# Performance work log

Measured on AMD Instinct MI355X. Metric: run time of the kernel, lower is better.

Reference implementation:

```python
import jax, jax.numpy as jnp
import numpy as np
import math

L = 16
LOGT = 19
T = 2 ** LOGT
F = 2
NMIN = 16
NMAX = 2048
X_MIN = 0.0
X_MAX = 1.0
N_POINTS = 524288
P1 = np.uint32(2654435761)  # spatial hash prime for y
P2 = np.uint32(805459861)   # spatial hash prime for z


def setup_inputs() -> dict:
    key = jax.random.key(0)
    k1, k2 = jax.random.split(key)
    x = jax.random.uniform(k1, (N_POINTS, 3), dtype=jnp.float32)
    hashmap = jax.random.normal(k2, (L, T, F), dtype=jnp.float32) * 1e-2
    b = math.exp((math.log(NMAX) - math.log(NMIN)) / (L - 1))
    resolution = jnp.asarray(np.floor(NMIN * b ** np.arange(L)), dtype=jnp.float32)
    return {"x": x, "hashmap": hashmap, "resolution": resolution}


def reference(x, hashmap, resolution):
    # normalize coords to [0,1] (x_min=0, x_max=1 here)
    xn = (x - X_MIN) / (X_MAX - X_MIN)
    # per-level scaled coords: [L, n, 3]
    xs = xn[None, :, :] * resolution[:, None, None]
    x0f = jnp.floor(xs)
    w = xs - x0f                                 # trilinear weights [L, n, 3]
    c0 = x0f.astype(jnp.uint32)
    c1 = c0 + jnp.uint32(1)
    hx0, hy0, hz0 = c0[..., 0], c0[..., 1] * P1, c0[..., 2] * P2
    hx1, hy1, hz1 = c1[..., 0], c1[..., 1] * P1, c1[..., 2] * P2
    Tm = jnp.uint32(T - 1)
    # 8 corner hash indices, order 000,001,010,011,100,101,110,111: [L, n, 8]
    idx = jnp.stack([
        (hx0 ^ hy0 ^ hz0) & Tm, (hx0 ^ hy0 ^ hz1) & Tm,
        (hx0 ^ hy1 ^ hz0) & Tm, (hx0 ^ hy1 ^ hz1) & Tm,
        (hx1 ^ hy0 ^ hz0) & Tm, (hx1 ^ hy0 ^ hz1) & Tm,
        (hx1 ^ hy1 ^ hz0) & Tm, (hx1 ^ hy1 ^ hz1) & Tm,
    ], axis=-1).astype(jnp.int32)
    wx, wy, wz = w[..., 0], w[..., 1], w[..., 2]
    wxn, wyn, wzn = 1.0 - wx, 1.0 - wy, 1.0 - wz
    # corner weights matching idx order: [L, n, 8]
    cw = jnp.stack([
        wxn * wyn * wzn, wxn * wyn * wz, wxn * wy * wzn, wxn * wy * wz,
        wx * wyn * wzn, wx * wyn * wz, wx * wy * wzn, wx * wy * wz,
    ], axis=-1)
    # gather per-level corner features: [L, n, 8, F]
    feats = jax.vmap(lambda h, i: h[i])(hashmap, idx)
    # interpolate and lay out as [n, L*F] (level-major, matching kernel store)
    out = jnp.einsum('lnc,lncf->nlf', cw, feats)
    return out.reshape(x.shape[0], L * F)
```

## Files before the change

kernel.cpp:

```cpp
#include <hip/hip_runtime.h>

namespace {
constexpr unsigned kT  = 1u << 19;
constexpr unsigned kTm = kT - 1u;
constexpr unsigned kP1 = 2654435761u;
constexpr unsigned kP2 = 805459861u;
constexpr int      kNPTS = 524288;

constexpr int      kD[3]    = {17, 23, 31};
constexpr unsigned kC[3]    = {17u*17u*17u, 23u*23u*23u, 31u*31u*31u};
constexpr unsigned kBase[3] = {0u, kC[0]*8u, (kC[0]+kC[1])*8u};
constexpr unsigned kTotElems = (kC[0]+kC[1]+kC[2])*8u;
constexpr size_t   kStageOff   = (size_t)4u << 20;
constexpr size_t   kStageBytes = (size_t)kNPTS * 16u * 8u;
constexpr size_t   kWsNeed     = kStageOff + kStageBytes;

constexpr int kNSeg[8]      = {5,2,3,3,2,3,3,2};
constexpr int kSegLvl[8][5] = {
  {0,1,2,3,4}, {4,5,0,0,0}, {5,6,7,0,0}, {7,8,9,0,0},
  {9,10,0,0,0}, {10,11,12,0,0}, {12,13,14,0,0}, {14,15,0,0,0}};
constexpr int kSegBeg[8][5] = {
  {0,0,0,0,0}, {26,0,0,0,0}, {1485,0,0,0,0}, {896,0,0,0,0},
  {307,0,0,0,0}, {1766,0,0,0,0}, {1177,0,0,0,0}, {589,0,0,0,0}};
constexpr int kSegEnd[8][5] = {
  {2048,2048,2048,2048,26}, {2048,1485,0,0,0}, {2048,2048,896,0,0},
  {2048,2048,307,0,0}, {2048,1766,0,0,0}, {2048,2048,1177,0,0},
  {2048,2048,589,0,0}, {2048,2048,0,0,0}};
constexpr unsigned kMaxBlk = 8218;
}

typedef float f32x2 __attribute__((ext_vector_type(2)));
typedef float f32x4 __attribute__((ext_vector_type(4)));

__global__ __launch_bounds__(256) void build_dense(
    const float* __restrict__ hashmap, f32x2* __restrict__ dense)
{
    unsigned t = blockIdx.x * 256 + threadIdx.x;
    if (t >= kTotElems) return;
    int l; unsigned rem;
    if (t < kC[0]*8u)              { l = 0; rem = t; }
    else if (t < (kC[0]+kC[1])*8u) { l = 1; rem = t - kC[0]*8u; }
    else                           { l = 2; rem = t - (kC[0]+kC[1])*8u; }
    unsigned cell = rem >> 3, corner = rem & 7u;
    unsigned D = (unsigned)kD[l];
    unsigned ck = cell % D, tmp = cell / D;
    unsigned cj = tmp % D,  ci = tmp / D;
    unsigned ii = ci + ((corner >> 2) & 1u);
    unsigned jj = cj + ((corner >> 1) & 1u);
    unsigned kk = ck + (corner & 1u);
    unsigned h = (ii ^ (jj * kP1) ^ (kk * kP2)) & kTm;
    dense[t] = reinterpret_cast<const f32x2*>(hashmap)[(size_t)l * kT + h];
}

__global__ __launch_bounds__(256) void hashgrid_gather(
    const float* __restrict__ x,
    const float* __restrict__ hashmap,
    const float* __restrict__ resolution,
    const f32x2* __restrict__ dense,
    f32x2* __restrict__ stage)
{
    unsigned i = blockIdx.x;
    unsigned g = i & 7u;
    unsigned j = i >> 3;

    int lvl = -1; unsigned chunk = 0, acc = 0;
    #pragma unroll
    for (int s = 0; s < 5; ++s) {
        if (s >= kNSeg[g]) break;
        unsigned len = (unsigned)(kSegEnd[g][s] - kSegBeg[g][s]);
        if (j < acc + len) { lvl = kSegLvl[g][s]; chunk = kSegBeg[g][s] + (j - acc); break; }
        acc += len;
    }
    if (lvl < 0) return;

    int n = (int)(chunk * 256u + threadIdx.x);

    float px = __builtin_nontemporal_load(&x[3*n+0]);
    float py = __builtin_nontemporal_load(&x[3*n+1]);
    float pz = __builtin_nontemporal_load(&x[3*n+2]);
    float res = resolution[lvl];

    float xs = px*res, ys = py*res, zs = pz*res;
    float fx = floorf(xs), fy = floorf(ys), fz = floorf(zs);
    float wx = xs-fx, wy = ys-fy, wz = zs-fz;

    unsigned cx0 = (unsigned)fx;
    unsigned cy0 = (unsigned)fy;
    unsigned cz0 = (unsigned)fz;

    f32x2 f000, f001, f010, f011, f100, f101, f110, f111;

    if (lvl < 3) {
        unsigned D = (unsigned)kD[lvl];
        size_t cellIdx = ((size_t)cx0 * D + cy0) * D + cz0;
        const f32x4* blk = reinterpret_cast<const f32x4*>(
            dense + kBase[lvl] + cellIdx * 8u);
        f32x4 q0 = blk[0], q1 = blk[1], q2 = blk[2], q3 = blk[3];
        f000 = {q0.x,q0.y}; f001 = {q0.z,q0.w};
        f010 = {q1.x,q1.y}; f011 = {q1.z,q1.w};
        f100 = {q2.x,q2.y}; f101 = {q2.z,q2.w};
        f110 = {q3.x,q3.y}; f111 = {q3.z,q3.w};
    } else {
        unsigned hy0 = cy0 * kP1, hy1 = (cy0 + 1u) * kP1;
        unsigned hz0 = cz0 * kP2, hz1 = (cz0 + 1u) * kP2;
        unsigned hyz00 = hy0 ^ hz0, hyz01 = hy0 ^ hz1;
        unsigned hyz10 = hy1 ^ hz0, hyz11 = hy1 ^ hz1;
        const f32x2* __restrict__ tb =
            reinterpret_cast<const f32x2*>(hashmap) + (size_t)lvl * kT;

        if ((cx0 & 1u) == 0u) {
            const f32x4* __restrict__ tb4 = reinterpret_cast<const f32x4*>(tb);
            unsigned i00 = (cx0 ^ hyz00) & kTm;
            unsigned i01 = (cx0 ^ hyz01) & kTm;
            unsigned i10 = (cx0 ^ hyz10) & kTm;
            unsigned i11 = (cx0 ^ hyz11) & kTm;
            f32x4 q00 = tb4[i00 >> 1];
            f32x4 q01 = tb4[i01 >> 1];
            f32x4 q10 = tb4[i10 >> 1];
            f32x4 q11 = tb4[i11 >> 1];
            bool o0 = (i00 & 1u), o1 = (i01 & 1u), o2 = (i10 & 1u), o3 = (i11 & 1u);
            f000.x = o0 ? q00.z : q00.x; f000.y = o0 ? q00.w : q00.y;
            f100.x = o0 ? q00.x : q00.z; f100.y = o0 ? q00.y : q00.w;
            f001.x = o1 ? q01.z : q01.x; f001.y = o1 ? q01.w : q01.y;
            f101.x = o1 ? q01.x : q01.z; f101.y = o1 ? q01.y : q01.w;
            f010.x = o2 ? q10.z : q10.x; f010.y = o2 ? q10.w : q10.y;
            f110.x = o2 ? q10.x : q10.z; f110.y = o2 ? q10.y : q10.w;
            f011.x = o3 ? q11.z : q11.x; f011.y = o3 ? q11.w : q11.y;
            f111.x = o3 ? q11.x : q11.z; f111.y = o3 ? q11.y : q11.w;
        } else {
            unsigned hx0 = cx0, hx1 = cx0 + 1u;
            f000 = tb[(hx0 ^ hyz00) & kTm];
            f001 = tb[(hx0 ^ hyz01) & kTm];
            f010 = tb[(hx0 ^ hyz10) & kTm];
            f011 = tb[(hx0 ^ hyz11) & kTm];
            f100 = tb[(hx1 ^ hyz00) & kTm];
            f101 = tb[(hx1 ^ hyz01) & kTm];
            f110 = tb[(hx1 ^ hyz10) & kTm];
            f111 = tb[(hx1 ^ hyz11) & kTm];
        }
    }

    float wxn = 1.f - wx, wyn = 1.f - wy, wzn = 1.f - wz;
    float w000 = wxn*wyn*wzn, w001 = wxn*wyn*wz;
    float w010 = wxn*wy *wzn, w011 = wxn*wy *wz;
    float w100 = wx *wyn*wzn, w101 = wx *wyn*wz;
    float w110 = wx *wy *wzn, w111 = wx *wy *wz;

    f32x2 o;
    o.x = w000*f000.x + w001*f001.x + w010*f010.x + w011*f011.x
        + w100*f100.x + w101*f101.x + w110*f110.x + w111*f111.x;
    o.y = w000*f000.y + w001*f001.y + w010*f010.y + w011*f011.y
        + w100*f100.y + w101*f101.y + w110*f110.y + w111*f111.y;

    __builtin_nontemporal_store(o, &stage[(size_t)lvl * kNPTS + n]);
}

__global__ __launch_bounds__(256) void stage_transpose(
    const f32x2* __restrict__ stage, f32x4* __restrict__ out4)
{
    __shared__ f32x2 tile[128][17];
    unsigned n0 = blockIdx.x * 128u;
    unsigned t = threadIdx.x;

    #pragma unroll
    for (int it = 0; it < 8; ++it) {
        unsigned m = (unsigned)it * 256u + t;
        unsigned l = m >> 7, p = m & 127u;
        tile[p][l] = stage[(size_t)l * kNPTS + n0 + p];
    }
    __syncthreads();

    #pragma unroll
    for (int it = 0; it < 4; ++it) {
        unsigned v = (unsigned)it * 256u + t;
        unsigned p = v >> 3, q = v & 7u;
        f32x2 a = tile[p][2u*q], b = tile[p][2u*q + 1u];
        f32x4 w; w.x = a.x; w.y = a.y; w.z = b.x; w.w = b.y;
        __builtin_nontemporal_store(w, &out4[(size_t)(n0 + p) * 8u + q]);
    }
}

__global__ __launch_bounds__(256) void hashgrid_fwd_lvl(
    const float* __restrict__ x,
    const float* __restrict__ hashmap,
    const float* __restrict__ resolution,
    f32x2* __restrict__ out,
    int npts, unsigned cpl)
{
    unsigned i = blockIdx.x;
    unsigned g = i & 7u;
    unsigned j = i >> 3;
    unsigned phase = j / cpl;
    unsigned chunk = j - phase * cpl;
    unsigned l = g + (phase << 3);

    int n = (int)(chunk * 256u + threadIdx.x);
    if (n >= npts) return;

    float px = x[3*n+0], py = x[3*n+1], pz = x[3*n+2];
    float res = resolution[l];

    float xs = px*res, ys = py*res, zs = pz*res;
    float fx = floorf(xs), fy = floorf(ys), fz = floorf(zs);
    float wx = xs-fx, wy = ys-fy, wz = zs-fz;

    unsigned cx0 = (unsigned)fx, cy0 = (unsigned)fy, cz0 = (unsigned)fz;
    unsigned hx0 = cx0,       hx1 = cx0 + 1u;
    unsigned hy0 = cy0 * kP1, hy1 = (cy0 + 1u) * kP1;
    unsigned hz0 = cz0 * kP2, hz1 = (cz0 + 1u) * kP2;

    const f32x2* __restrict__ tb =
        reinterpret_cast<const f32x2*>(hashmap) + (size_t)l * kT;
    f32x2 f000 = tb[(hx0 ^ hy0 ^ hz0) & kTm];
    f32x2 f001 = tb[(hx0 ^ hy0 ^ hz1) & kTm];
    f32x2 f010 = tb[(hx0 ^ hy1 ^ hz0) & kTm];
    f32x2 f011 = tb[(hx0 ^ hy1 ^ hz1) & kTm];
    f32x2 f100 = tb[(hx1 ^ hy0 ^ hz0) & kTm];
    f32x2 f101 = tb[(hx1 ^ hy0 ^ hz1) & kTm];
    f32x2 f110 = tb[(hx1 ^ hy1 ^ hz0) & kTm];
    f32x2 f111 = tb[(hx1 ^ hy1 ^ hz1) & kTm];

    float wxn = 1.f - wx, wyn = 1.f - wy, wzn = 1.f - wz;
    float w000 = wxn*wyn*wzn, w001 = wxn*wyn*wz;
    float w010 = wxn*wy *wzn, w011 = wxn*wy *wz;
    float w100 = wx *wyn*wzn, w101 = wx *wyn*wz;
    float w110 = wx *wy *wzn, w111 = wx *wy *wz;

    f32x2 o;
    o.x = w000*f000.x + w001*f001.x + w010*f010.x + w011*f011.x
        + w100*f100.x + w101*f101.x + w110*f110.x + w111*f111.x;
    o.y = w000*f000.y + w001*f001.y + w010*f010.y + w011*f011.y
        + w100*f100.y + w101*f101.y + w110*f110.y + w111*f111.y;

    __builtin_nontemporal_store(o, &out[(size_t)n*16 + l]);
}

extern "C" void kernel_launch(void* const* d_in, const int* in_sizes, int n_in,
                              void* d_out, int out_size, void* d_ws, size_t ws_size,
                              hipStream_t stream) {
    const float* x          = (const float*)d_in[0];
    const float* hashmap    = (const float*)d_in[1];
    const float* resolution = (const float*)d_in[2];

    int npts = in_sizes[0] / 3;

    if (npts == kNPTS && d_ws != nullptr && ws_size >= kWsNeed) {
        f32x2* dense = (f32x2*)d_ws;
        f32x2* stage = (f32x2*)((char*)d_ws + kStageOff);
        unsigned pb = (kTotElems + 255u) / 256u;
        build_dense<<<pb, 256, 0, stream>>>(hashmap, dense);
        hashgrid_gather<<<8u * kMaxBlk, 256, 0, stream>>>(
            x, hashmap, resolution, dense, stage);
        stage_transpose<<<kNPTS / 128, 256, 0, stream>>>(
            stage, (f32x4*)d_out);
    } else {
        unsigned cpl = (unsigned)((npts + 255) / 256);
        unsigned blocks = 16u * cpl;
        hashgrid_fwd_lvl<<<blocks, 256, 0, stream>>>(
            x, hashmap, resolution, (f32x2*)d_out, npts, cpl);
    }
}
```

Before: 241.1 us.

## Store dense corner tables in fp16 and extend dense path to level 3

Result: no change. 242.8 us (+0.7%).

```diff
diff --git a/kernel.cpp b/kernel.cpp
--- a/kernel.cpp
+++ b/kernel.cpp
@@ -1,4 +1,5 @@
 #include <hip/hip_runtime.h>
+#include <hip/hip_fp16.h>
 
 namespace {
 constexpr unsigned kT  = 1u << 19;
@@ -7,56 +8,68 @@
 constexpr unsigned kP2 = 805459861u;
 constexpr int      kNPTS = 524288;
 
-constexpr int      kD[3]    = {17, 23, 31};
-constexpr unsigned kC[3]    = {17u*17u*17u, 23u*23u*23u, 31u*31u*31u};
-constexpr unsigned kBase[3] = {0u, kC[0]*8u, (kC[0]+kC[1])*8u};
-constexpr unsigned kTotElems = (kC[0]+kC[1]+kC[2])*8u;
-constexpr size_t   kStageOff   = (size_t)4u << 20;
-constexpr size_t   kStageBytes = (size_t)kNPTS * 16u * 8u;
-constexpr size_t   kWsNeed     = kStageOff + kStageBytes;
-
-constexpr int kNSeg[8]      = {5,2,3,3,2,3,3,2};
-constexpr int kSegLvl[8][5] = {
-  {0,1,2,3,4}, {4,5,0,0,0}, {5,6,7,0,0}, {7,8,9,0,0},
-  {9,10,0,0,0}, {10,11,12,0,0}, {12,13,14,0,0}, {14,15,0,0,0}};
-constexpr int kSegBeg[8][5] = {
-  {0,0,0,0,0}, {26,0,0,0,0}, {1485,0,0,0,0}, {896,0,0,0,0},
-  {307,0,0,0,0}, {1766,0,0,0,0}, {1177,0,0,0,0}, {589,0,0,0,0}};
-constexpr int kSegEnd[8][5] = {
-  {2048,2048,2048,2048,26}, {2048,1485,0,0,0}, {2048,2048,896,0,0},
-  {2048,2048,307,0,0}, {2048,1766,0,0,0}, {2048,2048,1177,0,0},
-  {2048,2048,589,0,0}, {2048,2048,0,0,0}};
-constexpr unsigned kMaxBlk = 8218;
-}
-
-typedef float f32x2 __attribute__((ext_vector_type(2)));
-typedef float f32x4 __attribute__((ext_vector_type(4)));
-
-__global__ __launch_bounds__(256) void build_dense(
-    const float* __restrict__ hashmap, f32x2* __restrict__ dense)
+constexpr int      kD[4]        = {17, 23, 31, 43};
+constexpr unsigned kCells[4]    = {17u*17u*17u, 23u*23u*23u, 31u*31u*31u, 43u*43u*43u};
+constexpr unsigned kCellBase[4] = {0u, 4913u, 17080u, 46871u};
+constexpr unsigned kTotCells    = 126378u;
+constexpr unsigned kDenseElems  = kTotCells * 8u;
+constexpr size_t   kStageOff    = (size_t)4u << 20;
+constexpr size_t   kStageBytes  = (size_t)kNPTS * 16u * 8u;
+constexpr size_t   kWsNeed      = kStageOff + kStageBytes;
+
+constexpr int kNSeg[8]      = {4,3,3,2,2,3,3,2};
+constexpr int kSegLvl[8][4] = {
+  {0,1,2,3}, {3,4,5,0}, {5,6,7,0}, {7,8,0,0},
+  {9,10,0,0}, {10,11,12,0}, {12,13,14,0}, {14,15,0,0}};
+constexpr int kSegBeg[8][4] = {
+  {0,0,0,0}, {1024,0,0,0}, {1024,0,0,0}, {512,0,0,0},
+  {0,0,0,0}, {1536,0,0,0}, {1024,0,0,0}, {512,0,0,0}};
+constexpr int kSegEnd[8][4] = {
+  {2048,2048,2048,1024}, {2048,2048,1024,0}, {2048,2048,512,0}, {2048,2048,0,0},
+  {2048,1536,0,0}, {2048,2048,1024,0}, {2048,2048,512,0}, {2048,2048,0,0}};
+constexpr unsigned kMaxBlk = 7168;
+}
+
+typedef float    f32x2 __attribute__((ext_vector_type(2)));
+typedef float    f32x4 __attribute__((ext_vector_type(4)));
+typedef unsigned u32x4 __attribute__((ext_vector_type(4)));
+
+__device__ inline f32x2 h2_to_f2(unsigned w) {
+    __half2 h = __builtin_bit_cast(__half2, w);
+    f32x2 r; r.x = __half2float(h.x); r.y = __half2float(h.y);
+    return r;
+}
+
+__global__ __launch_bounds__(256) void build_dense16(
+    const float* __restrict__ hashmap, unsigned* __restrict__ dense16)
 {
     unsigned t = blockIdx.x * 256 + threadIdx.x;
-    if (t >= kTotElems) return;
+    if (t >= kDenseElems) return;
+    unsigned cell = t >> 3, corner = t & 7u;
     int l; unsigned rem;
-    if (t < kC[0]*8u)              { l = 0; rem = t; }
-    else if (t < (kC[0]+kC[1])*8u) { l = 1; rem = t - kC[0]*8u; }
-    else                           { l = 2; rem = t - (kC[0]+kC[1])*8u; }
-    unsigned cell = rem >> 3, corner = rem & 7u;
+    if      (cell < kCellBase[1]) { l = 0; rem = cell; }
+    else if (cell < kCellBase[2]) { l = 1; rem = cell - kCellBase[1]; }
+    else if (cell < kCellBase[3]) { l = 2; rem = cell - kCellBase[2]; }
+    else                          { l = 3; rem = cell - kCellBase[3]; }
     unsigned D = (unsigned)kD[l];
-    unsigned ck = cell % D, tmp = cell / D;
+    unsigned ck = rem % D, tmp = rem / D;
     unsigned cj = tmp % D,  ci = tmp / D;
     unsigned ii = ci + ((corner >> 2) & 1u);
     unsigned jj = cj + ((corner >> 1) & 1u);
     unsigned kk = ck + (corner & 1u);
     unsigned h = (ii ^ (jj * kP1) ^ (kk * kP2)) & kTm;
-    dense[t] = reinterpret_cast<const f32x2*>(hashmap)[(size_t)l * kT + h];
+    f32x2 v = reinterpret_cast<const f32x2*>(hashmap)[(size_t)l * kT + h];
+    __half2 p;
+    p.x = __float2half_rn(v.x);
+    p.y = __float2half_rn(v.y);
+    dense16[t] = __builtin_bit_cast(unsigned, p);
 }
 
 __global__ __launch_bounds__(256) void hashgrid_gather(
     const float* __restrict__ x,
     const float* __restrict__ hashmap,
     const float* __restrict__ resolution,
-    const f32x2* __restrict__ dense,
+    const unsigned* __restrict__ dense16,
     f32x2* __restrict__ stage)
 {
     unsigned i = blockIdx.x;
@@ -65,7 +78,7 @@
 
     int lvl = -1; unsigned chunk = 0, acc = 0;
     #pragma unroll
-    for (int s = 0; s < 5; ++s) {
+    for (int s = 0; s < 4; ++s) {
         if (s >= kNSeg[g]) break;
         unsigned len = (unsigned)(kSegEnd[g][s] - kSegBeg[g][s]);
         if (j < acc + len) { lvl = kSegLvl[g][s]; chunk = kSegBeg[g][s] + (j - acc); break; }
@@ -90,16 +103,16 @@
 
     f32x2 f000, f001, f010, f011, f100, f101, f110, f111;
 
-    if (lvl < 3) {
+    if (lvl < 4) {
         unsigned D = (unsigned)kD[lvl];
-        size_t cellIdx = ((size_t)cx0 * D + cy0) * D + cz0;
-        const f32x4* blk = reinterpret_cast<const f32x4*>(
-            dense + kBase[lvl] + cellIdx * 8u);
-        f32x4 q0 = blk[0], q1 = blk[1], q2 = blk[2], q3 = blk[3];
-        f000 = {q0.x,q0.y}; f001 = {q0.z,q0.w};
-        f010 = {q1.x,q1.y}; f011 = {q1.z,q1.w};
-        f100 = {q2.x,q2.y}; f101 = {q2.z,q2.w};
-        f110 = {q3.x,q3.y}; f111 = {q3.z,q3.w};
+        unsigned cell = (cx0 * D + cy0) * D + cz0;
+        const u32x4* blk = reinterpret_cast<const u32x4*>(
+            dense16 + ((size_t)kCellBase[lvl] + cell) * 8u);
+        u32x4 lo = blk[0], hi = blk[1];
+        f000 = h2_to_f2(lo.x); f001 = h2_to_f2(lo.y);
+        f010 = h2_to_f2(lo.z); f011 = h2_to_f2(lo.w);
+        f100 = h2_to_f2(hi.x); f101 = h2_to_f2(hi.y);
+        f110 = h2_to_f2(hi.z); f111 = h2_to_f2(hi.w);
     } else {
         unsigned hy0 = cy0 * kP1, hy1 = (cy0 + 1u) * kP1;
         unsigned hz0 = cz0 * kP2, hz1 = (cz0 + 1u) * kP2;
@@ -245,12 +258,12 @@
     int npts = in_sizes[0] / 3;
 
     if (npts == kNPTS && d_ws != nullptr && ws_size >= kWsNeed) {
-        f32x2* dense = (f32x2*)d_ws;
+        unsigned* dense16 = (unsigned*)d_ws;
         f32x2* stage = (f32x2*)((char*)d_ws + kStageOff);
-        unsigned pb = (kTotElems + 255u) / 256u;
-        build_dense<<<pb, 256, 0, stream>>>(hashmap, dense);
+        unsigned pb = (kDenseElems + 255u) / 256u;
+        build_dense16<<<pb, 256, 0, stream>>>(hashmap, dense16);
         hashgrid_gather<<<8u * kMaxBlk, 256, 0, stream>>>(
-            x, hashmap, resolution, dense, stage);
+            x, hashmap, resolution, dense16, stage);
         stage_transpose<<<kNPTS / 128, 256, 0, stream>>>(
             stage, (f32x4*)d_out);
     } else {
```
